# Kernel tuning notes

Measured on AMD Instinct MI355X. Metric: run time of the kernel, lower is better.

Reference implementation:

```python
import jax, jax.numpy as jnp
import numpy as np


def _time_encoding(t, hidden_dim):
    # Sinusoidal continuous-time encoding: t [B,T] -> [B,T,H]
    half = hidden_dim // 2
    freqs = jnp.exp(-jnp.arange(half, dtype=t.dtype) * (np.log(10000.0) / half))
    ang = t[..., None] * freqs  # [B,T,half]
    return jnp.concatenate([jnp.sin(ang), jnp.cos(ang)], axis=-1)


def _gru(x_tbh, w_ih, w_hh, b_ih, b_hh):
    # PyTorch-convention GRU over time-major input [T,B,H]
    B = x_tbh.shape[1]
    H = w_hh.shape[1]
    h0 = jnp.zeros((B, H), x_tbh.dtype)

    def step(h, x):
        gi = x @ w_ih.T + b_ih
        gh = h @ w_hh.T + b_hh
        i_r, i_z, i_n = jnp.split(gi, 3, axis=-1)
        h_r, h_z, h_n = jnp.split(gh, 3, axis=-1)
        r = jax.nn.sigmoid(i_r + h_r)
        z = jax.nn.sigmoid(i_z + h_z)
        n = jnp.tanh(i_n + r * h_n)
        h_new = (1.0 - z) * n + z * h
        return h_new, h_new

    _, ys = jax.lax.scan(step, h0, x_tbh)
    return ys  # [T,B,H]


def setup_inputs():
    key = jax.random.key(0)
    ks = jax.random.split(key, 8)
    B, T, D, H = 32, 256, 64, 128
    x = jax.random.normal(ks[0], (B, T, D), jnp.float32)
    missing_mask = (jax.random.uniform(ks[1], (B, T, D)) < 0.5).astype(jnp.float32)
    visit_time = jnp.cumsum(jax.random.uniform(ks[2], (B, T), jnp.float32) * 2.0, axis=1)
    time_delta = jnp.zeros((B, T), jnp.float32)
    lengths = jax.random.randint(ks[3], (B,), T // 2, T + 1).astype(jnp.int32)
    lengths = lengths.at[0].set(T)  # pad_packed returns max(lengths) steps; pin to T
    sensor_embed = jax.random.normal(ks[4], (D, H), jnp.float32) * 0.02
    k = 1.0 / np.sqrt(H)
    gru_w_ih = jax.random.uniform(ks[5], (3 * H, H), jnp.float32, -k, k)
    gru_w_hh = jax.random.uniform(ks[6], (3 * H, H), jnp.float32, -k, k)
    gru_b_ih = jax.random.uniform(ks[7], (3 * H,), jnp.float32, -k, k)
    gru_b_hh = jnp.zeros((3 * H,), jnp.float32)
    return dict(x=x, missing_mask=missing_mask, visit_time=visit_time,
                time_delta=time_delta, lengths=lengths, sensor_embed=sensor_embed,
                gru_w_ih=gru_w_ih, gru_w_hh=gru_w_hh, gru_b_ih=gru_b_ih, gru_b_hh=gru_b_hh)


def reference(x, missing_mask, visit_time, time_delta, lengths, sensor_embed,
              gru_w_ih, gru_w_hh, gru_b_ih, gru_b_hh):
    B, T, D = x.shape
    H = sensor_embed.shape[1]
    observed = 1.0 - missing_mask                                   # [B,T,D]
    # sensor tokens: per-(t,sensor) embedding scaled by value, zeroed if missing
    sensor_tokens = x[..., None] * sensor_embed[None, None] * observed[..., None]  # [B,T,D,H]
    presence = observed.mean(axis=1)                                # [B,D]
    sim = jax.nn.relu(sensor_embed @ sensor_embed.T)                # [D,D]
    adj = presence[:, :, None] * presence[:, None, :] * sim[None]   # [B,D,D]
    adj = adj + jnp.eye(D, dtype=x.dtype)[None]
    adj = adj / jnp.maximum(adj.sum(axis=-1, keepdims=True), 1e-6)
    graph_tokens = jnp.einsum('bij,btjh->btih', adj, sensor_tokens) # [B,T,D,H]
    visit_repr = graph_tokens.mean(axis=2) + _time_encoding(visit_time, H)  # [B,T,H]
    # dropout is identity in eval mode
    ys = _gru(jnp.swapaxes(visit_repr, 0, 1), gru_w_ih, gru_w_hh, gru_b_ih, gru_b_hh)
    out = jnp.swapaxes(ys, 0, 1)                                    # [B,T,H]
    # pad_packed_sequence semantics: zeros beyond each sequence length
    mask = (jnp.arange(T)[None, :] < lengths[:, None])[..., None]
    return out * mask
```

## Files before the change

### kernel.cpp

```cpp
#include <hip/hip_runtime.h>
#include <hip/hip_bf16.h>

#define B_ 32
#define T_ 256
#define D_ 64
#define H_ 128
#define G_ 384

typedef _Float16 half8 __attribute__((ext_vector_type(8)));
typedef _Float16 half4v __attribute__((ext_vector_type(4)));
typedef _Float16 half2v __attribute__((ext_vector_type(2)));
typedef float float4v __attribute__((ext_vector_type(4)));

__device__ __forceinline__ float fsigmoid(float x){ return 1.0f/(1.0f+__expf(-x)); }
__device__ __forceinline__ float ftanh_(float x){ return 1.0f - 2.0f/(1.0f+__expf(2.0f*x)); }

#define BAR() do{ asm volatile("s_waitcnt lgkmcnt(0)" ::: "memory"); \
                  __builtin_amdgcn_s_barrier(); \
                  asm volatile("" ::: "memory"); } while(0)

__global__ void __launch_bounds__(256) adj_k(const float* mm, const float* E,
                                             float* wcol){
  int b = blockIdx.x;
  int tid = threadIdx.x;
  int d = tid & 63, q = tid >> 6;
  __shared__ float spp[4][64];
  __shared__ float sp[64];
  __shared__ float sE[64*129];
  __shared__ float ssim[64*65];
  __shared__ float srs[64];
  float p = 0.0f;
  for (int t = q*64; t < q*64+64; t++) p += 1.0f - mm[(b*T_ + t)*D_ + d];
  spp[q][d] = p;
  for (int i = tid; i < D_*H_; i += 256){ int r = i >> 7, c = i & 127; sE[r*129+c] = E[i]; }
  __syncthreads();
  if (tid < 64) sp[tid] = (spp[0][tid]+spp[1][tid]+spp[2][tid]+spp[3][tid]) * (1.0f/T_);
  __syncthreads();
  float rowE[128];
  #pragma unroll
  for (int k = 0; k < 128; k++) rowE[k] = sE[d*129+k];
  for (int i = q*16; i < q*16+16; i++){
    float s = 0.0f;
    #pragma unroll
    for (int k = 0; k < 128; k++) s += rowE[k]*sE[i*129+k];
    ssim[d*65+i] = fmaxf(s, 0.0f);
  }
  __syncthreads();
  if (tid < 64){
    float rs = 0.0f;
    for (int j = 0; j < 64; j++) rs += sp[j]*ssim[tid*65+j];
    srs[tid] = fmaxf(sp[tid]*rs + 1.0f, 1e-6f);
  }
  __syncthreads();
  if (tid < 64){
    float s = 0.0f;
    for (int i = 0; i < 64; i++) s += sp[i]*ssim[tid*65+i]/srs[i];
    wcol[b*64 + tid] = sp[tid]*s + 1.0f/srs[tid];
  }
}

#define AVP 72
#define VRP 136
#define SEP 132
__global__ void __launch_bounds__(512,1) gi_k(const float* x, const float* mm,
                                              const float* vt, const float* E,
                                              const float* wih, const float* bih,
                                              const float* bhh, const float* wcol,
                                              _Float16* gi3){
  int bid = blockIdx.x;
  int b = bid >> 3, t0 = (bid & 7)*32;
  int tid = threadIdx.x;
  int w = tid >> 6, l = tid & 63;
  int lq = l >> 4, lm = l & 15;

  __shared__ __align__(16) _Float16 av[32*AVP];
  __shared__ __align__(16) _Float16 vrA[32*VRP];
  __shared__ __align__(16) _Float16 sEl[64*SEP];
  __shared__ float sVt[32];

  {
    int i = tid*4, t = i >> 6, d4 = i & 63;
    long src = (long)(b*T_ + t0 + t)*D_ + d4;
    float4 xv = *(const float4*)&x[src];
    float4 mv = *(const float4*)&mm[src];
    float4 wv = *(const float4*)&wcol[b*D_ + d4];
    half4v h;
    h[0]=(_Float16)(xv.x*(1.0f-mv.x)*wv.x*(1.0f/64));
    h[1]=(_Float16)(xv.y*(1.0f-mv.y)*wv.y*(1.0f/64));
    h[2]=(_Float16)(xv.z*(1.0f-mv.z)*wv.z*(1.0f/64));
    h[3]=(_Float16)(xv.w*(1.0f-mv.w)*wv.w*(1.0f/64));
    *(half4v*)&av[t*AVP + d4] = h;
  }
  {
    int r = tid >> 3, c0 = (tid & 7)*16;
    #pragma unroll
    for (int g = 0; g < 4; g++){
      float4 v = *(const float4*)&E[r*H_ + c0 + g*4];
      half4v h;
      h[0]=(_Float16)v.x; h[1]=(_Float16)v.y; h[2]=(_Float16)v.z; h[3]=(_Float16)v.w;
      *(half4v*)&sEl[r*SEP + c0 + g*4] = h;
    }
  }
  if (tid < 32) sVt[tid] = vt[b*T_ + t0 + tid];
  __syncthreads();

  half8 bE[2];
  #pragma unroll
  for (int kc = 0; kc < 2; kc++){
    half8 f;
    #pragma unroll
    for (int jj = 0; jj < 8; jj++)
      f[jj] = sEl[(kc*32 + lq*8 + jj)*SEP + 16*w + lm];
    bE[kc] = f;
  }

  float4v accA[2] = {{0,0,0,0},{0,0,0,0}};
  #pragma unroll
  for (int kc = 0; kc < 2; kc++){
    #pragma unroll
    for (int mt = 0; mt < 2; mt++){
      half8 a = *(const half8*)&av[(mt*16+lm)*AVP + kc*32 + lq*8];
      accA[mt] = __builtin_amdgcn_mfma_f32_16x16x32_f16(a, bE[kc], accA[mt], 0,0,0);
    }
  }
  {
    int h = 16*w + lm;
    float fr = __expf(-(float)(h & 63) * 0.14391157f);
    #pragma unroll
    for (int mt = 0; mt < 2; mt++){
      #pragma unroll
      for (int r = 0; r < 4; r++){
        int tl = mt*16 + lq*4 + r;
        float ang = sVt[tl] * fr;
        float e = (h < 64) ? __sinf(ang) : __cosf(ang);
        vrA[tl*VRP + h] = (_Float16)(accA[mt][r] + e);
      }
    }
  }
  __syncthreads();

  half8 bW[3][4]; float biW[3];
  #pragma unroll
  for (int q = 0; q < 3; q++){
    int g = 16*(3*w + q) + lm;
    biW[q] = bih[g] + (g < 2*H_ ? bhh[g] : 0.0f);
    #pragma unroll
    for (int kc = 0; kc < 4; kc++){
      const float* src = &wih[(long)g*H_ + kc*32 + lq*8];
      float4 x0 = *(const float4*)src;
      float4 x1 = *(const float4*)(src+4);
      half8 f;
      f[0]=(_Float16)x0.x; f[1]=(_Float16)x0.y; f[2]=(_Float16)x0.z; f[3]=(_Float16)x0.w;
      f[4]=(_Float16)x1.x; f[5]=(_Float16)x1.y; f[6]=(_Float16)x1.z; f[7]=(_Float16)x1.w;
      bW[q][kc] = f;
    }
  }
  float4v cB[2][3];
  #pragma unroll
  for (int mt = 0; mt < 2; mt++)
    #pragma unroll
    for (int q = 0; q < 3; q++) cB[mt][q] = (float4v){0,0,0,0};
  #pragma unroll
  for (int kc = 0; kc < 4; kc++){
    #pragma unroll
    for (int mt = 0; mt < 2; mt++){
      half8 a = *(const half8*)&vrA[(mt*16+lm)*VRP + kc*32 + lq*8];
      #pragma unroll
      for (int q = 0; q < 3; q++)
        cB[mt][q] = __builtin_amdgcn_mfma_f32_16x16x32_f16(a, bW[q][kc], cB[mt][q], 0,0,0);
    }
  }
  #pragma unroll
  for (int mt = 0; mt < 2; mt++){
    #pragma unroll
    for (int q = 0; q < 3; q++){
      int g = 16*(3*w + q) + lm;
      int tb = t0 + mt*16 + lq*4;
      half4v hv;
      hv[0]=(_Float16)(cB[mt][q][0] + biW[q]); hv[1]=(_Float16)(cB[mt][q][1] + biW[q]);
      hv[2]=(_Float16)(cB[mt][q][2] + biW[q]); hv[3]=(_Float16)(cB[mt][q][3] + biW[q]);
      *(half4v*)&gi3[((long)(b*G_ + g))*T_ + tb] = hv;
    }
  }
}

__global__ void __launch_bounds__(256,1) gru_k(const _Float16* gi3, const float* whh,
                                               const float* bhh, const int* lengths,
                                               float* out){
  int b = blockIdx.x;
  int tid = threadIdx.x;
  int w = tid >> 6, l = tid & 63;
  int kh = l >> 5;
  int j  = 32*w + (l & 31);
  bool lo = (kh == 0);
  int len = lengths[b];

  __shared__ __align__(16) _Float16 hb[2][H_];

  half2v Wr[32], Wz[32], Wn[32];
  {
    const float* baseR = &whh[(long)j*H_        + kh*64];
    const float* baseZ = &whh[(long)(H_ + j)*H_ + kh*64];
    const float* baseN = &whh[(long)(2*H_+j)*H_ + kh*64];
    #pragma unroll
    for (int t4 = 0; t4 < 16; t4++){
      float4 vr = *(const float4*)(baseR + t4*4);
      float4 vz = *(const float4*)(baseZ + t4*4);
      float4 vn = *(const float4*)(baseN + t4*4);
      half2v a;
      a[0]=(_Float16)vr.x; a[1]=(_Float16)vr.y; Wr[2*t4] = a;
      a[0]=(_Float16)vr.z; a[1]=(_Float16)vr.w; Wr[2*t4+1] = a;
      a[0]=(_Float16)vz.x; a[1]=(_Float16)vz.y; Wz[2*t4] = a;
      a[0]=(_Float16)vz.z; a[1]=(_Float16)vz.w; Wz[2*t4+1] = a;
      a[0]=(_Float16)vn.x; a[1]=(_Float16)vn.y; Wn[2*t4] = a;
      a[0]=(_Float16)vn.z; a[1]=(_Float16)vn.w; Wn[2*t4+1] = a;
    }
  }
  float bn_ = bhh[2*H_ + j];
  const _Float16* pr = gi3 + ((long)b*G_ + j)*T_;
  const _Float16* pz = pr + (long)H_*T_;
  const _Float16* pn = pr + (long)2*H_*T_;

  if (tid < H_){ hb[0][tid] = (_Float16)0.0f; hb[1][tid] = (_Float16)0.0f; }

  half8 prA, pzA, pnA, prB, pzB, pnB;
  if (lo){
    prA = *(const half8*)pr; pzA = *(const half8*)pz; pnA = *(const half8*)pn;
  }
  __syncthreads();

  float hval = 0.0f;

  auto substeps = [&](half8 cr, half8 cz, half8 cn, int c){
    float ho[8];
    #pragma unroll
    for (int i = 0; i < 8; i++){
      const int rp = i & 1;
      float ar0=0.0f, ar1=0.0f, az0=0.0f, az1=0.0f, an0=0.0f, an1=0.0f;
      #pragma unroll
      for (int q8 = 0; q8 < 8; q8++){
        half8 hv = *(const half8*)&hb[rp][kh*64 + q8*8];
        #pragma unroll
        for (int m = 0; m < 4; m++){
          half2v h2; h2[0] = hv[2*m]; h2[1] = hv[2*m+1];
          const int q = q8*4 + m;
          if ((q & 1) == 0){
            ar0 = __builtin_amdgcn_fdot2(h2, Wr[q], ar0, false);
            az0 = __builtin_amdgcn_fdot2(h2, Wz[q], az0, false);
            an0 = __builtin_amdgcn_fdot2(h2, Wn[q], an0, false);
          } else {
            ar1 = __builtin_amdgcn_fdot2(h2, Wr[q], ar1, false);
            az1 = __builtin_amdgcn_fdot2(h2, Wz[q], az1, false);
            an1 = __builtin_amdgcn_fdot2(h2, Wn[q], an1, false);
          }
        }
      }
      float R = ar0 + ar1, Z = az0 + az1, N = an0 + an1;
      R += __shfl_xor(R, 32, 64);
      Z += __shfl_xor(Z, 32, 64);
      N += __shfl_xor(N, 32, 64);
      if (lo){
        float r = fsigmoid((float)cr[i] + R);
        float z = fsigmoid((float)cz[i] + Z);
        float n = ftanh_((float)cn[i] + r*(N + bn_));
        hval = (1.0f - z)*n + z*hval;
        hb[rp^1][j] = (_Float16)hval;
        ho[i] = (c*8 + i < len) ? hval : 0.0f;
      }
      BAR();
    }
    if (lo){
      long ob = ((long)b*T_ + c*8)*H_ + j;
      #pragma unroll
      for (int i = 0; i < 8; i++) out[ob + (long)i*H_] = ho[i];
    }
  };

  for (int c = 0; c < 32; c += 2){
    if (lo){
      int nb = (c+1)*8;
      prB = *(const half8*)(pr+nb); pzB = *(const half8*)(pz+nb); pnB = *(const half8*)(pn+nb);
    }
    substeps(prA, pzA, pnA, c);
    if (lo && c+2 < 32){
      int nb = (c+2)*8;
      prA = *(const half8*)(pr+nb); pzA = *(const half8*)(pz+nb); pnA = *(const half8*)(pn+nb);
    }
    substeps(prB, pzB, pnB, c+1);
  }
}

extern "C" void kernel_launch(void* const* d_in, const int* in_sizes, int n_in,
                              void* d_out, int out_size, void* d_ws, size_t ws_size,
                              hipStream_t stream) {
  char* base = (char*)d_ws;
  size_t off = 0;
  auto alloc = [&](size_t bytes)->void*{
    void* p = base + off; off = (off + bytes + 255) & ~(size_t)255; return p;
  };
  float*     wcol = (float*)alloc((size_t)B_*D_*4);
  _Float16*  gi3  = (_Float16*)alloc((size_t)B_*G_*T_*2);
  if (off > ws_size) return;

  const float* x   = (const float*)d_in[0];
  const float* mm  = (const float*)d_in[1];
  const float* vt  = (const float*)d_in[2];
  const int*   len = (const int*)d_in[4];
  const float* E   = (const float*)d_in[5];
  const float* wih = (const float*)d_in[6];
  const float* whh = (const float*)d_in[7];
  const float* bih = (const float*)d_in[8];
  const float* bhh = (const float*)d_in[9];

  adj_k<<<dim3(B_),dim3(256),0,stream>>>(mm, E, wcol);
  gi_k<<<dim3(256),dim3(512),0,stream>>>(x, mm, vt, E, wih, bih, bhh, wcol, gi3);
  gru_k<<<dim3(B_),dim3(256),0,stream>>>(gi3, whh, bhh, len, (float*)d_out);
}
```

Baseline: 264.4 us.

## Split GRU recurrent matvec over four K-slices with 512-thread blocks

The recurrent GRU kernel now uses 512 threads per batch row. Each hidden unit's dot product is split into four 32-element K-slices instead of two 64-element ones, and the partial sums are reduced with two cross-lane shuffles. This halves the per-thread serial fdot2 chain on each timestep's critical path and halves the weight registers per thread. The cost is an extra shuffle stage and a barrier across 8 waves instead of 4. Output stores now go out every timestep rather than being batched per 8 steps.

```diff
diff --git a/kernel.cpp b/kernel.cpp
--- a/kernel.cpp
+++ b/kernel.cpp
@@ -184,26 +184,26 @@
   }
 }
 
-__global__ void __launch_bounds__(256,1) gru_k(const _Float16* gi3, const float* whh,
+__global__ void __launch_bounds__(512,1) gru_k(const _Float16* gi3, const float* whh,
                                                const float* bhh, const int* lengths,
                                                float* out){
   int b = blockIdx.x;
   int tid = threadIdx.x;
   int w = tid >> 6, l = tid & 63;
-  int kh = l >> 5;
-  int j  = 32*w + (l & 31);
-  bool lo = (kh == 0);
+  int kq = l >> 4;
+  int j  = 16*w + (l & 15);
+  bool g0 = (kq == 0);
   int len = lengths[b];
 
   __shared__ __align__(16) _Float16 hb[2][H_];
 
-  half2v Wr[32], Wz[32], Wn[32];
+  half2v Wr[16], Wz[16], Wn[16];
   {
-    const float* baseR = &whh[(long)j*H_        + kh*64];
-    const float* baseZ = &whh[(long)(H_ + j)*H_ + kh*64];
-    const float* baseN = &whh[(long)(2*H_+j)*H_ + kh*64];
-    #pragma unroll
-    for (int t4 = 0; t4 < 16; t4++){
+    const float* baseR = &whh[(long)j*H_        + kq*32];
+    const float* baseZ = &whh[(long)(H_ + j)*H_ + kq*32];
+    const float* baseN = &whh[(long)(2*H_+j)*H_ + kq*32];
+    #pragma unroll
+    for (int t4 = 0; t4 < 8; t4++){
       float4 vr = *(const float4*)(baseR + t4*4);
       float4 vz = *(const float4*)(baseZ + t4*4);
       float4 vn = *(const float4*)(baseN + t4*4);
@@ -224,7 +224,7 @@
   if (tid < H_){ hb[0][tid] = (_Float16)0.0f; hb[1][tid] = (_Float16)0.0f; }
 
   half8 prA, pzA, pnA, prB, pzB, pnB;
-  if (lo){
+  if (g0){
     prA = *(const half8*)pr; pzA = *(const half8*)pz; pnA = *(const half8*)pn;
   }
   __syncthreads();
@@ -232,14 +232,13 @@
   float hval = 0.0f;
 
   auto substeps = [&](half8 cr, half8 cz, half8 cn, int c){
-    float ho[8];
     #pragma unroll
     for (int i = 0; i < 8; i++){
       const int rp = i & 1;
       float ar0=0.0f, ar1=0.0f, az0=0.0f, az1=0.0f, an0=0.0f, an1=0.0f;
       #pragma unroll
-      for (int q8 = 0; q8 < 8; q8++){
-        half8 hv = *(const half8*)&hb[rp][kh*64 + q8*8];
+      for (int q8 = 0; q8 < 4; q8++){
+        half8 hv = *(const half8*)&hb[rp][kq*32 + q8*8];
         #pragma unroll
         for (int m = 0; m < 4; m++){
           half2v h2; h2[0] = hv[2*m]; h2[1] = hv[2*m+1];
@@ -256,33 +255,32 @@
         }
       }
       float R = ar0 + ar1, Z = az0 + az1, N = an0 + an1;
+      R += __shfl_xor(R, 16, 64);
+      Z += __shfl_xor(Z, 16, 64);
+      N += __shfl_xor(N, 16, 64);
       R += __shfl_xor(R, 32, 64);
       Z += __shfl_xor(Z, 32, 64);
       N += __shfl_xor(N, 32, 64);
-      if (lo){
+      if (g0){
         float r = fsigmoid((float)cr[i] + R);
         float z = fsigmoid((float)cz[i] + Z);
         float n = ftanh_((float)cn[i] + r*(N + bn_));
         hval = (1.0f - z)*n + z*hval;
         hb[rp^1][j] = (_Float16)hval;
-        ho[i] = (c*8 + i < len) ? hval : 0.0f;
+        int t = c*8 + i;
+        out[((long)(b*T_ + t))*H_ + j] = (t < len) ? hval : 0.0f;
       }
       BAR();
     }
-    if (lo){
-      long ob = ((long)b*T_ + c*8)*H_ + j;
-      #pragma unroll
-      for (int i = 0; i < 8; i++) out[ob + (long)i*H_] = ho[i];
-    }
   };
 
   for (int c = 0; c < 32; c += 2){
-    if (lo){
+    if (g0){
       int nb = (c+1)*8;
       prB = *(const half8*)(pr+nb); pzB = *(const half8*)(pz+nb); pnB = *(const half8*)(pn+nb);
     }
     substeps(prA, pzA, pnA, c);
-    if (lo && c+2 < 32){
+    if (g0 && c+2 < 32){
       int nb = (c+2)*8;
       prA = *(const half8*)(pr+nb); pzA = *(const half8*)(pz+nb); pnA = *(const half8*)(pn+nb);
     }
@@ -314,5 +312,5 @@
 
   adj_k<<<dim3(B_),dim3(256),0,stream>>>(mm, E, wcol);
   gi_k<<<dim3(256),dim3(512),0,stream>>>(x, mm, vt, E, wih, bih, bhh, wcol, gi3);
-  gru_k<<<dim3(B_),dim3(256),0,stream>>>(gi3, whh, bhh, len, (float*)d_out);
+  gru_k<<<dim3(B_),dim3(512),0,stream>>>(gi3, whh, bhh, len, (float*)d_out);
 }
```

Result: slower. 277.2 us (+4.9%).
